# Performance work log

Hardware: AMD Instinct MI355X
Metric: run time of the kernel (lower is better)

## Reference

```python
import jax, jax.numpy as jnp
import numpy as np

# Config (matches init_kwargs)
T, B = 128, 32
I, H, O, G = 128, 320, 32, 8
GROUP = 16  # attn_group_size entries, 8 groups of 16 -> sums to I
DT, TAU_X, TAU_W = 0.02, 0.1, 0.2
ALPHA_X = DT / TAU_X          # 0.2
ALPHA_W = DT / TAU_W          # 0.1
E_PROP = 0.8


def _masks():
    e_h = int(E_PROP * H)  # 256
    # x2h: e_prop=1, zero_cols_prop=0, no diag removal -> all ones
    mask_x = jnp.ones((H, I), dtype=jnp.float32)
    # h2h: sign mask (+1 for E, -1 for I), diagonal zeroed
    sign_h = jnp.concatenate([jnp.ones(e_h), -jnp.ones(H - e_h)]).astype(jnp.float32)
    mask_h = jnp.tile(sign_h[None, :], (H, 1)) * (1.0 - jnp.eye(H, dtype=jnp.float32))
    # h2o: zero_cols = int(0.2*H) trailing columns removed, sign mask on the rest
    zc = int((1.0 - E_PROP) * H)  # 64
    exist = jnp.concatenate([jnp.ones(H - zc), jnp.zeros(zc)]).astype(jnp.float32)
    mask_o = jnp.tile((sign_h * exist)[None, :], (O, 1))
    # attn EILinear(H -> G): same column pattern as h2o
    mask_a = jnp.tile((sign_h * exist)[None, :], (G, 1))
    return mask_x, mask_h, mask_o, mask_a


def setup_inputs() -> dict:
    key = jax.random.key(0)
    ks = jax.random.split(key, 10)
    s = 0.05  # keep dynamics in a sane range
    return {
        "x": jax.random.normal(ks[0], (T, B, I), dtype=jnp.float32),
        "Rs": jax.random.uniform(ks[1], (T, B, 1), dtype=jnp.float32),
        "W_x2h": jax.random.normal(ks[2], (H, I), dtype=jnp.float32) * s,
        "W_h2h": jax.random.normal(ks[3], (H, H), dtype=jnp.float32) * s,
        "b_h2h": jax.random.normal(ks[4], (H,), dtype=jnp.float32) * s,
        "W_h2o": jax.random.normal(ks[5], (O, H), dtype=jnp.float32) * s,
        "b_h2o": jax.random.normal(ks[6], (O,), dtype=jnp.float32) * s,
        "W_attn": jax.random.normal(ks[7], (G, H), dtype=jnp.float32) * s,
        "b_attn": jax.random.normal(ks[8], (G,), dtype=jnp.float32) * s,
        "c_plas": jax.random.normal(ks[9], (6,), dtype=jnp.float32) * s,
    }


def reference(x, Rs, W_x2h, W_h2h, b_h2h, W_h2o, b_h2o, W_attn, b_attn, c_plas):
    mask_x, mask_h, mask_o, mask_a = _masks()
    relu = jax.nn.relu
    # effective (sign/existence constrained, positive) weights
    ew_attn = relu(W_attn) * mask_a                      # [G, H]
    ew_x0 = relu(W_x2h) * mask_x                         # [H, I]
    ew_h0 = relu(W_h2h) * mask_h                         # [H, H]
    c = jnp.abs(c_plas)

    state0 = jnp.zeros((B, H), dtype=x.dtype)            # x0=0, sigma_rec=0
    output0 = relu(state0)
    wx0 = jnp.broadcast_to(ew_x0[None], (B, H, I))       # batched fast weights
    wh0 = jnp.broadcast_to(ew_h0[None], (B, H, H))

    def step(carry, inp):
        state, output, wx, wh = carry
        x_t, R_t = inp                                   # [B,I], [B,1]
        # attention over hidden groups
        attn = jax.nn.softmax(output @ ew_attn.T + b_attn, axis=-1)  # [B,G]
        attn_full = jnp.repeat(attn, GROUP, axis=-1)     # [B,I]
        xm = x_t * attn_full * G
        # masked / positive-constrained fast weights applied per batch
        ewx = relu(wx) * mask_x[None]                    # [B,H,I]
        ewh = relu(wh) * mask_h[None]                    # [B,H,H]
        total = (jnp.einsum('bhi,bi->bh', ewx, xm)
                 + jnp.einsum('bhj,bj->bh', ewh, output) + b_h2h)
        new_state = state * (1.0 - ALPHA_X) + total * ALPHA_X
        new_output = jnp.tanh(relu(new_state))           # retanh
        # outer-product plasticity update
        R = R_t[:, :, None]                              # [B,1,1]
        wx_n = wx * (1.0 - ALPHA_W) + ALPHA_W * R * (
            c[0] * xm[:, None, :]
            + c[1] * new_output[:, :, None]
            + c[2] * jnp.einsum('bi,bj->bij', new_output, xm))
        wh_n = wh * (1.0 - ALPHA_W) + ALPHA_W * R * (
            c[3] * output[:, None, :]
            + c[4] * new_output[:, :, None]
            + c[5] * jnp.einsum('bi,bj->bij', new_output, output))
        return (new_state, new_output, wx_n, wh_n), new_output

    _, hs = jax.lax.scan(step, (state0, output0, wx0, wh0), (x, Rs))  # hs: [T,B,H]
    ew_o = relu(W_h2o) * mask_o                          # [O,H]
    out = jax.nn.sigmoid(jnp.einsum('tbh,oh->tbo', hs, ew_o) + b_h2o)
    return out, hs
```

## Files before the change

### kernel.cpp

```cpp
#include <hip/hip_runtime.h>

#define TT 128
#define BB 32
#define II 128
#define HH 320
#define OO 32
#define GG 8
#define HPAD 129

static __device__ __forceinline__ float fexp2(float x) { return __builtin_amdgcn_exp2f(x); }
static __device__ __forceinline__ float frcp(float x)  { return __builtin_amdgcn_rcpf(x); }

static __device__ __forceinline__ float tanh_pos(float x) {
    float e = fexp2(x * 2.8853900817779268f);
    return 1.0f - 2.0f * frcp(e + 1.0f);
}

__global__ __launch_bounds__(512, 2)
void leaky_rnn_kernel(const float* __restrict__ x, const float* __restrict__ Rs,
                      const float* __restrict__ Wx2h, const float* __restrict__ Wh2h,
                      const float* __restrict__ bh2h, const float* __restrict__ Wh2o,
                      const float* __restrict__ bh2o, const float* __restrict__ Wattn,
                      const float* __restrict__ battn, const float* __restrict__ cplas,
                      float* __restrict__ out, float* __restrict__ hs,
                      unsigned* __restrict__ ctr)
{
    const int tid  = threadIdx.x;
    const int bid  = blockIdx.x;
    const int b    = bid >> 3;
    const int sub  = bid & 7;
    const int w    = tid >> 6;
    const int lane = tid & 63;
    const int h0   = sub * 40;

    __shared__ float s_ea[GG * HH];
    __shared__ float s_out[2][HH];
    __shared__ float s_logit[GG];
    __shared__ float s_hist[40 * HPAD];
    __shared__ float s_hs[16 * HH];

    for (int idx = tid; idx < GG * HH; idx += 512) {
        int h = idx % HH;
        float m = (h < 256) ? 1.f : (h == 256 ? -1.f : 0.f);
        s_ea[idx] = fmaxf(Wattn[idx], 0.f) * m;
    }
    if (tid < HH) { s_out[0][tid] = 0.f; s_out[1][tid] = 0.f; }

    float wx[5][2], wh[5][5], st[5], bh[5];
    int hrow[5];
#pragma unroll
    for (int r = 0; r < 5; ++r) {
        int h = h0 + w * 5 + r;
        hrow[r] = h;
        bh[r] = bh2h[h];
        st[r] = 0.f;
#pragma unroll
        for (int c = 0; c < 2; ++c)
            wx[r][c] = fmaxf(Wx2h[h * II + lane + 64 * c], 0.f);
#pragma unroll
        for (int c = 0; c < 5; ++c) {
            int j = lane + 64 * c;
            float v = fmaxf(Wh2h[h * HH + j], 0.f);
            v = (c == 4) ? -v : v;
            wh[r][c] = (j == h) ? 0.f : v;
        }
    }
    float batt = battn[w];
    float c0 = fabsf(cplas[0]), c1 = fabsf(cplas[1]), c2 = fabsf(cplas[2]);
    float c3 = fabsf(cplas[3]), c4 = fabsf(cplas[4]), c5 = fabsf(cplas[5]);

    const float AX  = (float)(0.02 / 0.1);
    const float AW  = (float)(0.02 / 0.2);
    const float OMX = 1.f - AX;
    const float OMW = 1.f - AW;
    const float L2E = 1.4426950408889634f;

    __syncthreads();

    float xv0n = x[b * II + lane];
    float xv1n = x[b * II + lane + 64];
    float Rvn  = Rs[b];

#pragma unroll 1
    for (int t = 0; t < TT; ++t) {
        const float* so_cur = s_out[t & 1];
        float*       so_nxt = s_out[(t + 1) & 1];
        float xv0 = xv0n, xv1 = xv1n;
        float A   = AW * Rvn;

        float lp = 0.f;
#pragma unroll
        for (int k = 0; k < 5; ++k) {
            int hh2 = lane + 64 * k;
            lp = fmaf(s_ea[w * HH + hh2], so_cur[hh2], lp);
        }
#pragma unroll
        for (int m = 1; m < 64; m <<= 1) lp += __shfl_xor(lp, m, 64);
        if (lane == 0) s_logit[w] = lp + batt;
        __syncthreads();

        float lg[8];
#pragma unroll
        for (int g = 0; g < 8; ++g) lg[g] = s_logit[g];
        float mx = lg[0];
#pragma unroll
        for (int g = 1; g < 8; ++g) mx = fmaxf(mx, lg[g]);
        float se = 0.f, eg[8];
#pragma unroll
        for (int g = 0; g < 8; ++g) { eg[g] = fexp2((lg[g] - mx) * L2E); se += eg[g]; }
        float rinv = frcp(se);
        float xmc0 = xv0 * eg[lane >> 4] * 8.f * rinv;
        float xmc1 = xv1 * eg[(lane >> 4) + 4] * 8.f * rinv;

        float oc[5];
#pragma unroll
        for (int c = 0; c < 5; ++c) oc[c] = so_cur[lane + 64 * c];

        float p[5];
#pragma unroll
        for (int r = 0; r < 5; ++r) {
            int h = hrow[r];
            float pp = fmaxf(wx[r][0], 0.f) * xmc0;
            pp = fmaf(fmaxf(wx[r][1], 0.f), xmc1, pp);
#pragma unroll
            for (int c = 0; c < 5; ++c) {
                float wv = fmaxf(wh[r][c], 0.f);
                float so = (c == 4) ? -oc[4] : oc[c];
                float term = wv * so;
                term = ((lane + 64 * c) == h) ? 0.f : term;
                pp += term;
            }
            p[r] = pp;
        }
#pragma unroll
        for (int m = 1; m < 64; m <<= 1) {
#pragma unroll
            for (int r = 0; r < 5; ++r) p[r] += __shfl_xor(p[r], m, 64);
        }

        float no[5];
#pragma unroll
        for (int r = 0; r < 5; ++r) {
            float total = p[r] + bh[r];
            st[r] = fmaf(st[r], OMX, total * AX);
            no[r] = tanh_pos(fmaxf(st[r], 0.f));
        }

        {
            float pub = no[0];
            pub = (lane == 1) ? no[1] : pub;
            pub = (lane == 2) ? no[2] : pub;
            pub = (lane == 3) ? no[3] : pub;
            pub = (lane == 4) ? no[4] : pub;
            if (lane < 5) {
                __hip_atomic_store(&hs[(t * BB + b) * HH + h0 + w * 5 + lane], pub + 2.0f,
                                   __ATOMIC_RELAXED, __HIP_MEMORY_SCOPE_AGENT);
                s_hist[(w * 5 + lane) * HPAD + t] = pub;
            }
        }

        if (t < TT - 1) {
            float Ac0 = A * c0, Ac1 = A * c1, Ac2 = A * c2;
            float Ac3 = A * c3, Ac4 = A * c4, Ac5 = A * c5;
#pragma unroll
            for (int r = 0; r < 5; ++r) {
                float u  = fmaf(Ac2, no[r], Ac0);
                float v  = Ac1 * no[r];
                float pp = fmaf(Ac5, no[r], Ac3);
                float qq = Ac4 * no[r];
                wx[r][0] = fmaf(wx[r][0], OMW, fmaf(u, xmc0, v));
                wx[r][1] = fmaf(wx[r][1], OMW, fmaf(u, xmc1, v));
#pragma unroll
                for (int c = 0; c < 5; ++c)
                    wh[r][c] = fmaf(wh[r][c], OMW, fmaf(pp, oc[c], qq));
            }
        }

        if (t + 1 < TT) {
            xv0n = x[((t + 1) * BB + b) * II + lane];
            xv1n = x[((t + 1) * BB + b) * II + lane + 64];
            Rvn  = Rs[(t + 1) * BB + b];
        }

        if (t < TT - 1 && tid < HH) {
            const float* p2 = &hs[(t * BB + b) * HH + tid];
            float va = __hip_atomic_load(p2, __ATOMIC_RELAXED, __HIP_MEMORY_SCOPE_AGENT);
            float vb = __hip_atomic_load(p2, __ATOMIC_RELAXED, __HIP_MEMORY_SCOPE_AGENT);
            float vc = __hip_atomic_load(p2, __ATOMIC_RELAXED, __HIP_MEMORY_SCOPE_AGENT);
            float vd = __hip_atomic_load(p2, __ATOMIC_RELAXED, __HIP_MEMORY_SCOPE_AGENT);
            int guard = 0;
            while (va < 1.0f && ++guard < 2000000) {
                va = vb; vb = vc; vc = vd;
                vd = __hip_atomic_load(p2, __ATOMIC_RELAXED, __HIP_MEMORY_SCOPE_AGENT);
            }
            so_nxt[tid] = va - 2.0f;
        }
        __syncthreads();
    }

    if (tid == 0) {
        __hip_atomic_fetch_add(&ctr[b * 32], 1u, __ATOMIC_RELAXED, __HIP_MEMORY_SCOPE_AGENT);
        int guard = 0;
        while (__hip_atomic_load(&ctr[b * 32], __ATOMIC_RELAXED, __HIP_MEMORY_SCOPE_AGENT) < 8u) {
            if (++guard > 2000000) break;
            __builtin_amdgcn_s_sleep(1);
        }
    }
    __syncthreads();

    for (int idx = tid; idx < 16 * HH; idx += 512) {
        int tl = idx / HH, h = idx % HH;
        int t_g = sub * 16 + tl;
        s_hs[idx] = __hip_atomic_load(&hs[(t_g * BB + b) * HH + h],
                                      __ATOMIC_RELAXED, __HIP_MEMORY_SCOPE_AGENT) - 2.0f;
    }
    __syncthreads();
    {
        int t_loc = tid >> 5;
        int o     = tid & 31;
        int t_g   = sub * 16 + t_loc;
        const float* hp = &s_hs[t_loc * HH];
        float acc = bh2o[o];
#pragma unroll 4
        for (int h = 0; h < 257; ++h) {
            float m = (h == 256) ? -1.f : 1.f;
            acc = fmaf(fmaxf(Wh2o[o * HH + h], 0.f) * m, hp[h], acc);
        }
        float sg = frcp(1.f + fexp2(-acc * L2E));
        out[(t_g * BB + b) * OO + o] = sg;
    }

    __syncthreads();
    if (tid == 0) {
        __hip_atomic_fetch_add(&ctr[b * 32], 1u, __ATOMIC_RELAXED, __HIP_MEMORY_SCOPE_AGENT);
        int guard = 0;
        while (__hip_atomic_load(&ctr[b * 32], __ATOMIC_RELAXED, __HIP_MEMORY_SCOPE_AGENT) < 16u) {
            if (++guard > 2000000) break;
            __builtin_amdgcn_s_sleep(1);
        }
    }
    __syncthreads();

    for (int idx = tid; idx < 40 * TT; idx += 512) {
        int row = idx >> 7;
        int t   = idx & 127;
        __hip_atomic_store(&hs[(t * BB + b) * HH + h0 + row], s_hist[row * HPAD + t],
                           __ATOMIC_RELAXED, __HIP_MEMORY_SCOPE_AGENT);
    }
}

extern "C" void kernel_launch(void* const* d_in, const int* in_sizes, int n_in,
                              void* d_out, int out_size, void* d_ws, size_t ws_size,
                              hipStream_t stream) {
    const float* x     = (const float*)d_in[0];
    const float* Rs    = (const float*)d_in[1];
    const float* Wx2h  = (const float*)d_in[2];
    const float* Wh2h  = (const float*)d_in[3];
    const float* bh2h  = (const float*)d_in[4];
    const float* Wh2o  = (const float*)d_in[5];
    const float* bh2o  = (const float*)d_in[6];
    const float* Wattn = (const float*)d_in[7];
    const float* battn = (const float*)d_in[8];
    const float* cplas = (const float*)d_in[9];
    float* out = (float*)d_out;
    float* hs  = out + TT * BB * OO;
    unsigned* ctr = (unsigned*)d_ws;

    hipMemsetAsync(d_ws, 0, 32 * 32 * sizeof(unsigned), stream);
    hipLaunchKernelGGL(leaky_rnn_kernel, dim3(256), dim3(512), 0, stream,
                       x, Rs, Wx2h, Wh2h, bh2h, Wh2o, bh2o, Wattn, battn, cplas,
                       out, hs, ctr);
}
```

Baseline: 502.2 us.

## Compute attention logits per wave in registers and use DPP reductions

Each wave now computes all 8 attention logits redundantly from weights held in registers, which removes the shared-memory logit exchange and one block-wide barrier per timestep. The wavefront reductions switch from shuffle-xor to DPP row operations plus a readlane broadcast. A block also writes its own hidden outputs straight into shared memory and skips polling global memory for them, and it pre-clears the next timestep's hs slot so the sentinel protocol still holds. The cost is much higher register pressure (launch bounds drop to one block per SIMD group) and redundant FLOPs in every wave.

```diff
diff --git a/kernel.cpp b/kernel.cpp
--- a/kernel.cpp
+++ b/kernel.cpp
@@ -16,7 +16,18 @@
     return 1.0f - 2.0f * frcp(e + 1.0f);
 }
 
-__global__ __launch_bounds__(512, 2)
+template<int CTRL>
+static __device__ __forceinline__ float dpp_add(float v) {
+    int t = __builtin_amdgcn_update_dpp(0, __builtin_bit_cast(int, v),
+                                        CTRL, 0xf, 0xf, true);
+    return v + __builtin_bit_cast(float, t);
+}
+static __device__ __forceinline__ float bcast63(float v) {
+    return __builtin_bit_cast(float,
+        __builtin_amdgcn_readlane(__builtin_bit_cast(int, v), 63));
+}
+
+__global__ __launch_bounds__(512, 1)
 void leaky_rnn_kernel(const float* __restrict__ x, const float* __restrict__ Rs,
                       const float* __restrict__ Wx2h, const float* __restrict__ Wh2h,
                       const float* __restrict__ bh2h, const float* __restrict__ Wh2o,
@@ -33,18 +44,23 @@
     const int lane = tid & 63;
     const int h0   = sub * 40;
 
-    __shared__ float s_ea[GG * HH];
     __shared__ float s_out[2][HH];
-    __shared__ float s_logit[GG];
     __shared__ float s_hist[40 * HPAD];
     __shared__ float s_hs[16 * HH];
 
-    for (int idx = tid; idx < GG * HH; idx += 512) {
-        int h = idx % HH;
-        float m = (h < 256) ? 1.f : (h == 256 ? -1.f : 0.f);
-        s_ea[idx] = fmaxf(Wattn[idx], 0.f) * m;
-    }
     if (tid < HH) { s_out[0][tid] = 0.f; s_out[1][tid] = 0.f; }
+
+    float ea_r[8][5], ba[8];
+#pragma unroll
+    for (int g = 0; g < 8; ++g) {
+        ba[g] = battn[g];
+#pragma unroll
+        for (int k = 0; k < 5; ++k) {
+            int j = lane + 64 * k;
+            float m = (j < 256) ? 1.f : (j == 256 ? -1.f : 0.f);
+            ea_r[g][k] = fmaxf(Wattn[g * HH + j], 0.f) * m;
+        }
+    }
 
     float wx[5][2], wh[5][5], st[5], bh[5];
     int hrow[5];
@@ -65,7 +81,6 @@
             wh[r][c] = (j == h) ? 0.f : v;
         }
     }
-    float batt = battn[w];
     float c0 = fabsf(cplas[0]), c1 = fabsf(cplas[1]), c2 = fabsf(cplas[2]);
     float c3 = fabsf(cplas[3]), c4 = fabsf(cplas[4]), c5 = fabsf(cplas[5]);
 
@@ -75,11 +90,15 @@
     const float OMW = 1.f - AW;
     const float L2E = 1.4426950408889634f;
 
-    __syncthreads();
-
     float xv0n = x[b * II + lane];
     float xv1n = x[b * II + lane + 64];
     float Rvn  = Rs[b];
+
+    if (lane < 5)
+        __hip_atomic_store(&hs[b * HH + h0 + w * 5 + lane], 0.0f,
+                           __ATOMIC_RELAXED, __HIP_MEMORY_SCOPE_AGENT);
+
+    __syncthreads();
 
 #pragma unroll 1
     for (int t = 0; t < TT; ++t) {
@@ -88,20 +107,29 @@
         float xv0 = xv0n, xv1 = xv1n;
         float A   = AW * Rvn;
 
-        float lp = 0.f;
-#pragma unroll
-        for (int k = 0; k < 5; ++k) {
-            int hh2 = lane + 64 * k;
-            lp = fmaf(s_ea[w * HH + hh2], so_cur[hh2], lp);
-        }
-#pragma unroll
-        for (int m = 1; m < 64; m <<= 1) lp += __shfl_xor(lp, m, 64);
-        if (lane == 0) s_logit[w] = lp + batt;
-        __syncthreads();
+        float oc[5];
+#pragma unroll
+        for (int c = 0; c < 5; ++c) oc[c] = so_cur[lane + 64 * c];
 
         float lg[8];
 #pragma unroll
-        for (int g = 0; g < 8; ++g) lg[g] = s_logit[g];
+        for (int g = 0; g < 8; ++g) {
+            float lp = 0.f;
+#pragma unroll
+            for (int k = 0; k < 5; ++k) lp = fmaf(ea_r[g][k], oc[k], lp);
+            lg[g] = lp;
+        }
+#define DPP_L8(CTRL) { \
+        lg[0]=dpp_add<CTRL>(lg[0]); lg[1]=dpp_add<CTRL>(lg[1]); \
+        lg[2]=dpp_add<CTRL>(lg[2]); lg[3]=dpp_add<CTRL>(lg[3]); \
+        lg[4]=dpp_add<CTRL>(lg[4]); lg[5]=dpp_add<CTRL>(lg[5]); \
+        lg[6]=dpp_add<CTRL>(lg[6]); lg[7]=dpp_add<CTRL>(lg[7]); }
+        DPP_L8(0x111) DPP_L8(0x112) DPP_L8(0x114)
+        DPP_L8(0x118) DPP_L8(0x142) DPP_L8(0x143)
+#undef DPP_L8
+#pragma unroll
+        for (int g = 0; g < 8; ++g) lg[g] = bcast63(lg[g]) + ba[g];
+
         float mx = lg[0];
 #pragma unroll
         for (int g = 1; g < 8; ++g) mx = fmaxf(mx, lg[g]);
@@ -111,10 +139,6 @@
         float rinv = frcp(se);
         float xmc0 = xv0 * eg[lane >> 4] * 8.f * rinv;
         float xmc1 = xv1 * eg[(lane >> 4) + 4] * 8.f * rinv;
-
-        float oc[5];
-#pragma unroll
-        for (int c = 0; c < 5; ++c) oc[c] = so_cur[lane + 64 * c];
 
         float p[5];
 #pragma unroll
@@ -132,16 +156,18 @@
             }
             p[r] = pp;
         }
-#pragma unroll
-        for (int m = 1; m < 64; m <<= 1) {
-#pragma unroll
-            for (int r = 0; r < 5; ++r) p[r] += __shfl_xor(p[r], m, 64);
-        }
+#define DPP_L5(CTRL) { \
+        p[0]=dpp_add<CTRL>(p[0]); p[1]=dpp_add<CTRL>(p[1]); \
+        p[2]=dpp_add<CTRL>(p[2]); p[3]=dpp_add<CTRL>(p[3]); \
+        p[4]=dpp_add<CTRL>(p[4]); }
+        DPP_L5(0x111) DPP_L5(0x112) DPP_L5(0x114)
+        DPP_L5(0x118) DPP_L5(0x142) DPP_L5(0x143)
+#undef DPP_L5
 
         float no[5];
 #pragma unroll
         for (int r = 0; r < 5; ++r) {
-            float total = p[r] + bh[r];
+            float total = bcast63(p[r]) + bh[r];
             st[r] = fmaf(st[r], OMX, total * AX);
             no[r] = tanh_pos(fmaxf(st[r], 0.f));
         }
@@ -156,6 +182,10 @@
                 __hip_atomic_store(&hs[(t * BB + b) * HH + h0 + w * 5 + lane], pub + 2.0f,
                                    __ATOMIC_RELAXED, __HIP_MEMORY_SCOPE_AGENT);
                 s_hist[(w * 5 + lane) * HPAD + t] = pub;
+                so_nxt[h0 + w * 5 + lane] = pub;
+                if (t + 1 < TT)
+                    __hip_atomic_store(&hs[((t + 1) * BB + b) * HH + h0 + w * 5 + lane],
+                                       0.0f, __ATOMIC_RELAXED, __HIP_MEMORY_SCOPE_AGENT);
             }
         }
 
@@ -182,7 +212,7 @@
             Rvn  = Rs[(t + 1) * BB + b];
         }
 
-        if (t < TT - 1 && tid < HH) {
+        if (t < TT - 1 && tid < HH && !(tid >= h0 && tid < h0 + 40)) {
             const float* p2 = &hs[(t * BB + b) * HH + tid];
             float va = __hip_atomic_load(p2, __ATOMIC_RELAXED, __HIP_MEMORY_SCOPE_AGENT);
             float vb = __hip_atomic_load(p2, __ATOMIC_RELAXED, __HIP_MEMORY_SCOPE_AGENT);
```

New measurement: 484.6 us. 1.04x faster.
